# Optimization experiments

Measured on AMD Instinct MI355X. Metric: run time of the kernel, lower is better.

The kernel has to match this reference:

```python
import jax, jax.numpy as jnp
import numpy as np

N_NODES = 100000


def _gcn_conv(h, src, dst, norm, W, b, n):
    # linear transform then symmetric-normalized scatter-add aggregation
    hw = h @ W                                   # [N, out]
    msg = hw[src] * norm[:, None]                # [E+N, out] gathered messages
    out = jax.ops.segment_sum(msg, dst, num_segments=n)
    return out + b


def _self_loops_and_norm(edge_index, n):
    loop = jnp.arange(n, dtype=edge_index.dtype)
    src = jnp.concatenate([edge_index[0], loop])
    dst = jnp.concatenate([edge_index[1], loop])
    deg = jax.ops.segment_sum(jnp.ones_like(src, dtype=jnp.float32), dst, num_segments=n)
    dinv = jnp.where(deg > 0, jax.lax.rsqrt(jnp.maximum(deg, 1.0)), 0.0)
    norm = dinv[src] * dinv[dst]                 # D^-1/2 (A+I) D^-1/2 coefficients
    return src, dst, norm


def setup_inputs() -> dict:
    key = jax.random.key(0)
    k1, k2, k3, k4 = jax.random.split(key, 4)
    F_IN, H, C = 128, 64, 40
    x = jax.random.normal(k1, (N_NODES, F_IN), dtype=jnp.float32)
    edge_index = jax.random.randint(k2, (2, 3200000), 0, N_NODES, dtype=jnp.int64)
    s1 = 1.0 / np.sqrt(F_IN)
    s2 = 1.0 / np.sqrt(H)
    W1 = jax.random.uniform(k3, (F_IN, H), jnp.float32, -s1, s1)
    b1 = jnp.zeros((H,), jnp.float32)
    W2 = jax.random.uniform(k4, (H, C), jnp.float32, -s2, s2)
    b2 = jnp.zeros((C,), jnp.float32)
    return {"x": x, "edge_index": edge_index, "W1": W1, "b1": b1, "W2": W2, "b2": b2}


def reference(x, edge_index, W1, b1, W2, b2):
    n = x.shape[0]
    src, dst, norm = _self_loops_and_norm(edge_index, n)
    h = _gcn_conv(x, src, dst, norm, W1, b1, n)
    h = jax.nn.relu(h)
    # dropout(p=0.5) is identity in eval mode
    out = _gcn_conv(h, src, dst, norm, W2, b2, n)
    return jax.nn.log_softmax(out, axis=1)
```

## Files before the change

kernel.cpp:

```cpp
#include <hip/hip_runtime.h>
#include <math.h>

#define F_IN 128
#define HID  64
#define NCLS 40
#define PART_CHUNK 4096
#define CAP 4608
#define CAPX 768
#define MAXNB 1024
#define ASTRIDE 132
#define GSTRIDE 72

typedef _Float16 half8 __attribute__((ext_vector_type(8)));
typedef _Float16 half2t __attribute__((ext_vector_type(2)));
typedef float floatx4 __attribute__((ext_vector_type(4)));

__device__ inline half8 ld_half8_u8(const _Float16* p) {
    union { uint2 u[2]; half8 h; } r;
    r.u[0] = *(const uint2*)p;
    r.u[1] = *(const uint2*)(p + 4);
    return r.h;
}

__global__ __launch_bounds__(256) void fused_part_gemm1(const int* __restrict__ src,
                                                        const int* __restrict__ dst,
                                                        int* __restrict__ bCur,
                                                        int* __restrict__ pkBuf,
                                                        int E, int NB, int nPart,
                                                        const float* __restrict__ x,
                                                        const float* __restrict__ W1,
                                                        _Float16* __restrict__ h1, int n) {
    __shared__ __align__(16) char smem[2 * 64 * ASTRIDE * 2];
    int tid = threadIdx.x;
    if ((int)blockIdx.x < nPart) {
        int xcd = (int)blockIdx.x & 7;
        int* hcnt  = (int*)smem;
        int* hbase = (int*)smem + MAXNB;
        for (int i = tid; i < NB; i += 256) hcnt[i] = 0;
        __syncthreads();
        int e0 = blockIdx.x * PART_CHUNK;
        int s_[16], d_[16];
#pragma unroll
        for (int i = 0; i < 16; ++i) {
            int e = e0 + i * 256 + tid;
            if (e < E) {
                s_[i] = src[e]; d_[i] = dst[e];
                atomicAdd(&hcnt[d_[i] >> 7], 1);
            }
        }
        __syncthreads();
        for (int b = tid; b < NB; b += 256) {
            int c = hcnt[b];
            hbase[b] = c ? ((b * 8 + xcd) * CAPX + atomicAdd(&bCur[b * 8 + xcd], c)) : 0;
            hcnt[b] = 0;
        }
        __syncthreads();
#pragma unroll
        for (int i = 0; i < 16; ++i) {
            int e = e0 + i * 256 + tid;
            if (e < E) {
                int b = d_[i] >> 7;
                int loc = atomicAdd(&hcnt[b], 1);
                pkBuf[hbase[b] + loc] = (s_[i] << 7) | (d_[i] & 127);
            }
        }
    } else {
        _Float16* Ah = (_Float16*)smem;
        _Float16* Wt = Ah + 64 * ASTRIDE;
        int node0 = ((int)blockIdx.x - nPart) * 64;
#pragma unroll
        for (int i = 0; i < 8; ++i) {
            int f = (i * 256 + tid) * 4;
            int m = f >> 7, k = f & 127;
            float4 v = (node0 + m < n) ? ((const float4*)(x + (size_t)(node0 + m) * F_IN))[k >> 2]
                                       : make_float4(0.f, 0.f, 0.f, 0.f);
            _Float16* p = &Ah[m * ASTRIDE + k];
            p[0] = (_Float16)v.x; p[1] = (_Float16)v.y; p[2] = (_Float16)v.z; p[3] = (_Float16)v.w;
        }
#pragma unroll
        for (int i = 0; i < 32; ++i) {
            int f = i * 256 + tid;
            int k = f >> 6, nn = f & 63;
            Wt[nn * ASTRIDE + k] = (_Float16)W1[f];
        }
        __syncthreads();
        int wave = tid >> 6, lane = tid & 63;
        int m0 = wave * 16;
        int col = lane & 15, quad = lane >> 4;
        floatx4 acc[4] = {{0,0,0,0},{0,0,0,0},{0,0,0,0},{0,0,0,0}};
#pragma unroll
        for (int kk = 0; kk < 4; ++kk) {
            int kbase = kk * 32 + quad * 8;
            half8 a = ld_half8_u8(&Ah[(m0 + col) * ASTRIDE + kbase]);
#pragma unroll
            for (int t = 0; t < 4; ++t) {
                half8 b = ld_half8_u8(&Wt[(t * 16 + col) * ASTRIDE + kbase]);
                acc[t] = __builtin_amdgcn_mfma_f32_16x16x32_f16(a, b, acc[t], 0, 0, 0);
            }
        }
#pragma unroll
        for (int t = 0; t < 4; ++t)
#pragma unroll
            for (int r = 0; r < 4; ++r) {
                int node = node0 + m0 + quad * 4 + r;
                if (node < n) h1[(size_t)node * HID + t * 16 + col] = (_Float16)acc[t][r];
            }
    }
}

__global__ __launch_bounds__(256) void scan_buckets(const int* __restrict__ bCur,
                                                    int* __restrict__ bBase, int NB, int E) {
    __shared__ int part[256];
    int tid = threadIdx.x;
    int v[4]; int sum = 0;
#pragma unroll
    for (int k = 0; k < 4; ++k) {
        int i = tid * 4 + k;
        int s = 0;
        if (i < NB) {
#pragma unroll
            for (int x = 0; x < 8; ++x) s += bCur[i * 8 + x];
        }
        v[k] = s;
        sum += s;
    }
    part[tid] = sum; __syncthreads();
    for (int off = 1; off < 256; off <<= 1) {
        int t = (tid >= off) ? part[tid - off] : 0;
        __syncthreads();
        part[tid] += t;
        __syncthreads();
    }
    int base = part[tid] - sum;
#pragma unroll
    for (int k = 0; k < 4; ++k) {
        int i = tid * 4 + k;
        if (i < NB) bBase[i] = base;
        base += v[k];
    }
    if (tid == 255) bBase[NB] = E;
}

__global__ __launch_bounds__(256) void bucket_finalize(const int* __restrict__ bCur,
                                                       const int* __restrict__ bBase,
                                                       const int* __restrict__ pkBuf,
                                                       int* __restrict__ ptr,
                                                       float* __restrict__ dinv,
                                                       int* __restrict__ sIdx,
                                                       _Float16* __restrict__ h1,
                                                       int n, int E) {
    __shared__ int cnt128[128];
    __shared__ int sc[128];
    __shared__ int cur[128];
    __shared__ float sdinv[128];
    __shared__ int segoff[9];
    __shared__ int ebuf[CAP];
    __shared__ int stage[CAP];
    int b = blockIdx.x;
    int node0 = b << 7;
    int tid = threadIdx.x;
    if (tid < 128) cnt128[tid] = 0;
    if (tid == 0) {
        int o = 0;
#pragma unroll
        for (int x = 0; x < 8; ++x) { segoff[x] = o; o += bCur[b * 8 + x]; }
        segoff[8] = o;
    }
    __syncthreads();
    int cnt = segoff[8];
    int dbase = bBase[b];
    for (int x = 0; x < 8; ++x) {
        int off = segoff[x], len = segoff[x + 1] - off;
        const int* s = pkBuf + (size_t)(b * 8 + x) * CAPX;
        for (int j = tid; j < len; j += 256) {
            int p = s[j];
            ebuf[off + j] = p;
            atomicAdd(&cnt128[p & 127], 1);
        }
    }
    __syncthreads();
    int v = (tid < 128) ? cnt128[tid] : 0;
    if (tid < 128) sc[tid] = v;
    __syncthreads();
    for (int off = 1; off < 128; off <<= 1) {
        int t = (tid < 128 && tid >= off) ? sc[tid - off] : 0;
        __syncthreads();
        if (tid < 128) sc[tid] += t;
        __syncthreads();
    }
    if (tid < 128) {
        cur[tid] = sc[tid] - v;
        float dv = rsqrtf((float)v + 1.0f);
        sdinv[tid] = dv;
        int node = node0 + tid;
        if (node < n) {
            ptr[node] = dbase + sc[tid] - v;
            dinv[node] = dv;
        }
    }
    if (tid == 0 && b == gridDim.x - 1) ptr[n] = E;
    __syncthreads();
    for (int j = tid; j < cnt; j += 256) {
        int p = ebuf[j];
        int pos = atomicAdd(&cur[p & 127], 1);
        stage[pos] = p >> 7;
    }
    __syncthreads();
    for (int j = tid; j < cnt; j += 256)
        sIdx[dbase + j] = stage[j];
#pragma unroll
    for (int pass = 0; pass < 4; ++pass) {
        int idx = pass * 256 + tid;
        int nd = node0 + (idx >> 3);
        if (nd < n) {
            float dv = sdinv[idx >> 3];
            half8* p = (half8*)(h1 + (size_t)nd * HID) + (idx & 7);
            half8 hv = *p;
#pragma unroll
            for (int j = 0; j < 8; ++j) hv[j] = (_Float16)((float)hv[j] * dv);
            *p = hv;
        }
    }
}

template<bool RELU>
__global__ __launch_bounds__(256) void gather4(const int* __restrict__ ptr,
                                               const int* __restrict__ sIdx,
                                               const float* __restrict__ dinv,
                                               const _Float16* __restrict__ hin,
                                               const float* __restrict__ bias,
                                               _Float16* __restrict__ hout,
                                               const float* __restrict__ W2,
                                               const float* __restrict__ b2,
                                               float* __restrict__ out, int n) {
    __shared__ _Float16 gt[16 * GSTRIDE];
    __shared__ _Float16 wt[48 * GSTRIDE];
    int tid = threadIdx.x, wave = tid >> 6, lane = tid & 63;
    int ng   = lane >> 4;
    int slot = (lane >> 3) & 1;
    int fq   = lane & 7;
    int node = blockIdx.x * 16 + wave * 4 + ng;
    bool valid = node < n;
    int nodeC = valid ? node : 0;
    int beg = ptr[nodeC];
    int end = valid ? ptr[nodeC + 1] : beg;
    float di = dinv[nodeC];
    float a0[8] = {0,0,0,0,0,0,0,0}, a1[8] = {0,0,0,0,0,0,0,0};

    if (!RELU) {
#pragma unroll
        for (int i = 0; i < 12; ++i) {
            int f = i * 256 + tid;
            int c = f >> 6, k = f & 63;
            wt[c * GSTRIDE + k] = (c < NCLS) ? (_Float16)W2[k * NCLS + c] : (_Float16)0.f;
        }
    }

    if (slot == 0 && valid) {
        half8 v = *(const half8*)(hin + nodeC * HID + fq * 8);
#pragma unroll
        for (int j = 0; j < 8; ++j) a0[j] = (float)v[j];
    }
    const _Float16 ONE = (_Float16)1.0f, ZEROH = (_Float16)0.0f;
    if (beg < end) {
        int ja0 = beg + slot, jb0 = ja0 + 2, jc0 = ja0 + 4, jd0 = ja0 + 6;
        bool va = ja0 < end, vb = jb0 < end, vc = jc0 < end, vd = jd0 < end;
        int sa0 = sIdx[va ? ja0 : beg];
        int sb0 = sIdx[vb ? jb0 : beg];
        int sc0 = sIdx[vc ? jc0 : beg];
        int sd0 = sIdx[vd ? jd0 : beg];
        int ja1 = ja0 + 8, jb1 = jb0 + 8, jc1 = jc0 + 8, jd1 = jd0 + 8;
        bool va1 = ja1 < end, vb1 = jb1 < end, vc1 = jc1 < end, vd1 = jd1 < end;
        int sa1 = sIdx[va1 ? ja1 : beg];
        int sb1 = sIdx[vb1 ? jb1 : beg];
        int sc1 = sIdx[vc1 ? jc1 : beg];
        int sd1 = sIdx[vd1 ? jd1 : beg];
        half8 ra = *(const half8*)(hin + (size_t)sa0 * HID + fq * 8);
        half8 rb = *(const half8*)(hin + (size_t)sb0 * HID + fq * 8);
        half8 rc = *(const half8*)(hin + (size_t)sc0 * HID + fq * 8);
        half8 rd = *(const half8*)(hin + (size_t)sd0 * HID + fq * 8);
        for (int j0 = beg; j0 < end; j0 += 8) {
            half8 ra2 = *(const half8*)(hin + (size_t)sa1 * HID + fq * 8);
            half8 rb2 = *(const half8*)(hin + (size_t)sb1 * HID + fq * 8);
            half8 rc2 = *(const half8*)(hin + (size_t)sc1 * HID + fq * 8);
            half8 rd2 = *(const half8*)(hin + (size_t)sd1 * HID + fq * 8);
            int ja2 = j0 + 16 + slot, jb2 = ja2 + 2, jc2 = ja2 + 4, jd2 = ja2 + 6;
            bool va2 = ja2 < end, vb2 = jb2 < end, vc2 = jc2 < end, vd2 = jd2 < end;
            int sa2 = sIdx[va2 ? ja2 : beg];
            int sb2 = sIdx[vb2 ? jb2 : beg];
            int sc2 = sIdx[vc2 ? jc2 : beg];
            int sd2 = sIdx[vd2 ? jd2 : beg];
#if __has_builtin(__builtin_amdgcn_fdot2)
            half2t wab = { va ? ONE : ZEROH, vb ? ONE : ZEROH };
            half2t wcd = { vc ? ONE : ZEROH, vd ? ONE : ZEROH };
#pragma unroll
            for (int j = 0; j < 8; ++j) {
                half2t pab = { ra[j], rb[j] };
                half2t pcd = { rc[j], rd[j] };
                a0[j] = __builtin_amdgcn_fdot2(pab, wab, a0[j], false);
                a1[j] = __builtin_amdgcn_fdot2(pcd, wcd, a1[j], false);
            }
#else
            float wa = va ? 1.f : 0.f, wb = vb ? 1.f : 0.f, wc = vc ? 1.f : 0.f, wd = vd ? 1.f : 0.f;
#pragma unroll
            for (int j = 0; j < 8; ++j) {
                a0[j] = fmaf((float)ra[j], wa, a0[j]);
                a0[j] = fmaf((float)rb[j], wb, a0[j]);
                a1[j] = fmaf((float)rc[j], wc, a1[j]);
                a1[j] = fmaf((float)rd[j], wd, a1[j]);
            }
#endif
            ra = ra2; rb = rb2; rc = rc2; rd = rd2;
            va = va1; vb = vb1; vc = vc1; vd = vd1;
            sa1 = sa2; sb1 = sb2; sc1 = sc2; sd1 = sd2;
            va1 = va2; vb1 = vb2; vc1 = vc2; vd1 = vd2;
        }
    }
#pragma unroll
    for (int j = 0; j < 8; ++j) {
        a0[j] += a1[j];
        a0[j] += __shfl_xor(a0[j], 8, 64);
    }

    if (RELU) {
        if (slot == 0 && valid) {
            union { half8 h; uint4 u; } o;
#pragma unroll
            for (int j = 0; j < 8; ++j) {
                float v = di * a0[j];
                v = fmaxf(v + bias[fq * 8 + j], 0.f) * di;
                o.h[j] = (_Float16)v;
            }
            *(uint4*)(hout + nodeC * HID + fq * 8) = o.u;
        }
    } else {
        if (slot == 0) {
            int row = wave * 4 + ng;
#pragma unroll
            for (int j = 0; j < 8; ++j)
                gt[row * GSTRIDE + fq * 8 + j] = (_Float16)(di * a0[j]);
        }
        __syncthreads();
        if (wave == 0) {
            int col = lane & 15, quad = lane >> 4;
            floatx4 acc[3] = {{0,0,0,0},{0,0,0,0},{0,0,0,0}};
#pragma unroll
            for (int kk = 0; kk < 2; ++kk) {
                int kbase = kk * 32 + quad * 8;
                half8 a = *(const half8*)&gt[col * GSTRIDE + kbase];
#pragma unroll
                for (int t = 0; t < 3; ++t) {
                    half8 b = *(const half8*)&wt[(t * 16 + col) * GSTRIDE + kbase];
                    acc[t] = __builtin_amdgcn_mfma_f32_16x16x32_f16(a, b, acc[t], 0, 0, 0);
                }
            }
            float bb[3];
#pragma unroll
            for (int t = 0; t < 3; ++t) {
                int c = t * 16 + col;
                bb[t] = (c < NCLS) ? b2[c] : 0.f;
            }
            int nodeB = blockIdx.x * 16;
#pragma unroll
            for (int r = 0; r < 4; ++r) {
                int nd = nodeB + quad * 4 + r;
                float v0 = acc[0][r] + bb[0];
                float v1 = acc[1][r] + bb[1];
                float v2 = (col < 8) ? acc[2][r] + bb[2] : -INFINITY;
                float m = fmaxf(fmaxf(v0, v1), v2);
#pragma unroll
                for (int off = 1; off < 16; off <<= 1) m = fmaxf(m, __shfl_xor(m, off, 64));
                float s = expf(v0 - m) + expf(v1 - m) + ((col < 8) ? expf(v2 - m) : 0.f);
#pragma unroll
                for (int off = 1; off < 16; off <<= 1) s += __shfl_xor(s, off, 64);
                float ls = logf(s);
                if (nd < n) {
                    float* op = out + (size_t)nd * NCLS;
                    op[col]      = v0 - m - ls;
                    op[16 + col] = v1 - m - ls;
                    if (col < 8) op[32 + col] = v2 - m - ls;
                }
            }
        }
    }
}

extern "C" void kernel_launch(void* const* d_in, const int* in_sizes, int n_in,
                              void* d_out, int out_size, void* d_ws, size_t ws_size,
                              hipStream_t stream) {
    const float* x  = (const float*)d_in[0];
    const int*   ei = (const int*)d_in[1];
    const float* W1 = (const float*)d_in[2];
    const float* b1 = (const float*)d_in[3];
    const float* W2 = (const float*)d_in[4];
    const float* b2 = (const float*)d_in[5];
    float* out = (float*)d_out;

    int n = in_sizes[0] / F_IN;
    int E = in_sizes[1] / 2;
    const int* src = ei;
    const int* dst = ei + E;
    int NB = (n + 127) >> 7;
    int nPart = (E + PART_CHUNK - 1) / PART_CHUNK;
    int nGemm1 = (n + 63) / 64;

    char* ws = (char*)d_ws;
    const size_t MB = 1024 * 1024;
    int*      bCur  = (int*)  (ws);
    int*      bBase = (int*)  (ws + 64 * 1024);
    int*      ptr   = (int*)  (ws + 128 * 1024);
    float*    dinv  = (float*)(ws + 1 * MB);
    int*      sIdx  = (int*)     (ws + 2 * MB);
    _Float16* bufA  = (_Float16*)(ws + 15 * MB);
    int*      pkBuf = (int*)     (ws + 28 * MB);
    _Float16* bufB  = (_Float16*)(ws + 28 * MB);

    hipMemsetAsync(bCur, 0, (size_t)NB * 8 * sizeof(int), stream);
    fused_part_gemm1<<<nPart + nGemm1, 256, 0, stream>>>(src, dst, bCur, pkBuf, E, NB, nPart,
                                                         x, W1, bufA, n);
    scan_buckets<<<1, 256, 0, stream>>>(bCur, bBase, NB, E);
    bucket_finalize<<<NB, 256, 0, stream>>>(bCur, bBase, pkBuf, ptr, dinv, sIdx, bufA, n, E);

    gather4<true ><<<(n + 15) / 16, 256, 0, stream>>>(ptr, sIdx, dinv, bufA, b1, bufB,
                                                      W2, b2, out, n);
    gather4<false><<<(n + 15) / 16, 256, 0, stream>>>(ptr, sIdx, dinv, bufB, b1, bufB,
                                                      W2, b2, out, n);
}
```

Measured before the change: 297.9 us.

## Drop global bucket scan by using fixed-capacity CSR slots with explicit end pointers

The single-block scan_buckets kernel goes away. Each bucket now writes its sorted edges at a fixed offset b*CAP in sIdx and stores a per-node end pointer, so the gather kernels read ptr/pEnd instead of ptr[i+1]. The in-block 128-entry scan switches from a shared-memory Hillis-Steele loop to wave shuffles. This removes one serialized launch and several barriers, at the cost of a sparser sIdx layout (more workspace, gaps between buckets) and one extra index load per node.

```diff
diff --git a/kernel.cpp b/kernel.cpp
--- a/kernel.cpp
+++ b/kernel.cpp
@@ -108,43 +108,10 @@
     }
 }
 
-__global__ __launch_bounds__(256) void scan_buckets(const int* __restrict__ bCur,
-                                                    int* __restrict__ bBase, int NB, int E) {
-    __shared__ int part[256];
-    int tid = threadIdx.x;
-    int v[4]; int sum = 0;
-#pragma unroll
-    for (int k = 0; k < 4; ++k) {
-        int i = tid * 4 + k;
-        int s = 0;
-        if (i < NB) {
-#pragma unroll
-            for (int x = 0; x < 8; ++x) s += bCur[i * 8 + x];
-        }
-        v[k] = s;
-        sum += s;
-    }
-    part[tid] = sum; __syncthreads();
-    for (int off = 1; off < 256; off <<= 1) {
-        int t = (tid >= off) ? part[tid - off] : 0;
-        __syncthreads();
-        part[tid] += t;
-        __syncthreads();
-    }
-    int base = part[tid] - sum;
-#pragma unroll
-    for (int k = 0; k < 4; ++k) {
-        int i = tid * 4 + k;
-        if (i < NB) bBase[i] = base;
-        base += v[k];
-    }
-    if (tid == 255) bBase[NB] = E;
-}
-
 __global__ __launch_bounds__(256) void bucket_finalize(const int* __restrict__ bCur,
-                                                       const int* __restrict__ bBase,
                                                        const int* __restrict__ pkBuf,
                                                        int* __restrict__ ptr,
+                                                       int* __restrict__ pEnd,
                                                        float* __restrict__ dinv,
                                                        int* __restrict__ sIdx,
                                                        _Float16* __restrict__ h1,
@@ -168,7 +135,7 @@
     }
     __syncthreads();
     int cnt = segoff[8];
-    int dbase = bBase[b];
+    int dbase = b * CAP;
     for (int x = 0; x < 8; ++x) {
         int off = segoff[x], len = segoff[x + 1] - off;
         const int* s = pkBuf + (size_t)(b * 8 + x) * CAPX;
@@ -179,26 +146,33 @@
         }
     }
     __syncthreads();
-    int v = (tid < 128) ? cnt128[tid] : 0;
-    if (tid < 128) sc[tid] = v;
-    __syncthreads();
-    for (int off = 1; off < 128; off <<= 1) {
-        int t = (tid < 128 && tid >= off) ? sc[tid - off] : 0;
-        __syncthreads();
-        if (tid < 128) sc[tid] += t;
-        __syncthreads();
-    }
+    int v = 0;
+    if (tid < 128) {
+        v = cnt128[tid];
+        int vv = v;
+        int lane = tid & 63;
+#pragma unroll
+        for (int off = 1; off < 64; off <<= 1) {
+            int t = __shfl_up(vv, off, 64);
+            if (lane >= off) vv += t;
+        }
+        sc[tid] = vv;
+    }
+    __syncthreads();
+    if (tid >= 64 && tid < 128) sc[tid] += sc[63];
+    __syncthreads();
     if (tid < 128) {
         cur[tid] = sc[tid] - v;
         float dv = rsqrtf((float)v + 1.0f);
         sdinv[tid] = dv;
         int node = node0 + tid;
         if (node < n) {
-            ptr[node] = dbase + sc[tid] - v;
+            int p0 = dbase + sc[tid] - v;
+            ptr[node] = p0;
+            pEnd[node] = p0 + v;
             dinv[node] = dv;
         }
     }
-    if (tid == 0 && b == gridDim.x - 1) ptr[n] = E;
     __syncthreads();
     for (int j = tid; j < cnt; j += 256) {
         int p = ebuf[j];
@@ -225,6 +199,7 @@
 
 template<bool RELU>
 __global__ __launch_bounds__(256) void gather4(const int* __restrict__ ptr,
+                                               const int* __restrict__ pEnd,
                                                const int* __restrict__ sIdx,
                                                const float* __restrict__ dinv,
                                                const _Float16* __restrict__ hin,
@@ -243,7 +218,7 @@
     bool valid = node < n;
     int nodeC = valid ? node : 0;
     int beg = ptr[nodeC];
-    int end = valid ? ptr[nodeC + 1] : beg;
+    int end = valid ? pEnd[nodeC] : beg;
     float di = dinv[nodeC];
     float a0[8] = {0,0,0,0,0,0,0,0}, a1[8] = {0,0,0,0,0,0,0,0};
 
@@ -407,22 +382,21 @@
     char* ws = (char*)d_ws;
     const size_t MB = 1024 * 1024;
     int*      bCur  = (int*)  (ws);
-    int*      bBase = (int*)  (ws + 64 * 1024);
     int*      ptr   = (int*)  (ws + 128 * 1024);
+    int*      pEnd  = (int*)  (ws + 576 * 1024);
     float*    dinv  = (float*)(ws + 1 * MB);
     int*      sIdx  = (int*)     (ws + 2 * MB);
-    _Float16* bufA  = (_Float16*)(ws + 15 * MB);
-    int*      pkBuf = (int*)     (ws + 28 * MB);
-    _Float16* bufB  = (_Float16*)(ws + 28 * MB);
+    _Float16* bufA  = (_Float16*)(ws + 17 * MB);
+    int*      pkBuf = (int*)     (ws + 30 * MB);
+    _Float16* bufB  = (_Float16*)(ws + 30 * MB);
 
     hipMemsetAsync(bCur, 0, (size_t)NB * 8 * sizeof(int), stream);
     fused_part_gemm1<<<nPart + nGemm1, 256, 0, stream>>>(src, dst, bCur, pkBuf, E, NB, nPart,
                                                          x, W1, bufA, n);
-    scan_buckets<<<1, 256, 0, stream>>>(bCur, bBase, NB, E);
-    bucket_finalize<<<NB, 256, 0, stream>>>(bCur, bBase, pkBuf, ptr, dinv, sIdx, bufA, n, E);
-
-    gather4<true ><<<(n + 15) / 16, 256, 0, stream>>>(ptr, sIdx, dinv, bufA, b1, bufB,
+    bucket_finalize<<<NB, 256, 0, stream>>>(bCur, pkBuf, ptr, pEnd, dinv, sIdx, bufA, n, E);
+
+    gather4<true ><<<(n + 15) / 16, 256, 0, stream>>>(ptr, pEnd, sIdx, dinv, bufA, b1, bufB,
                                                       W2, b2, out, n);
-    gather4<false><<<(n + 15) / 16, 256, 0, stream>>>(ptr, sIdx, dinv, bufB, b1, bufB,
+    gather4<false><<<(n + 15) / 16, 256, 0, stream>>>(ptr, pEnd, sIdx, dinv, bufB, b1, bufB,
                                                       W2, b2, out, n);
 }
```

Result: no change. 293.7 us (-1.4%).
